# Kernel tuning notes

Hardware: AMD Instinct MI355X
Metric: run time of the kernel (lower is better)

Reference implementation:

```python
import jax, jax.numpy as jnp
import numpy as np

CROP_H = 14
CROP_W = 14
EXTRAPOLATION_VALUE = 0.0


def setup_inputs() -> dict:
    key = jax.random.key(0)
    k1, k2, k3 = jax.random.split(key, 3)
    image = jax.random.normal(k1, (8, 256, 100, 152), dtype=jnp.float32)
    # normalized box coords in [0,1]; (y1,x1,y2,x2), y2<y1 allowed (extrapolation handles it)
    boxes = jax.random.uniform(k2, (1000, 4), dtype=jnp.float32)
    box_ind = jax.random.randint(k3, (1000,), 0, 8, dtype=jnp.int32)
    return {"image": image, "boxes": boxes, "box_ind": box_ind}


def _crop_and_resize(image, boxes, box_ind):
    # image: [B, C, H, W]; boxes: [N, 4] (y1, x1, y2, x2) normalized; box_ind: [N]
    B, C, H, W = image.shape
    dt = image.dtype
    y1, x1, y2, x2 = boxes[:, 0], boxes[:, 1], boxes[:, 2], boxes[:, 3]

    # TF crop_and_resize sampling grid (crop size > 1 path)
    h_scale = (y2 - y1) * (H - 1) / (CROP_H - 1)          # [N]
    w_scale = (x2 - x1) * (W - 1) / (CROP_W - 1)          # [N]
    in_y = y1[:, None] * (H - 1) + jnp.arange(CROP_H, dtype=dt)[None, :] * h_scale[:, None]  # [N, ch]
    in_x = x1[:, None] * (W - 1) + jnp.arange(CROP_W, dtype=dt)[None, :] * w_scale[:, None]  # [N, cw]

    valid_y = (in_y >= 0) & (in_y <= H - 1)               # [N, ch]
    valid_x = (in_x >= 0) & (in_x <= W - 1)               # [N, cw]

    top = jnp.floor(in_y)
    left = jnp.floor(in_x)
    y_lerp = in_y - top                                    # [N, ch]
    x_lerp = in_x - left                                   # [N, cw]

    ti = jnp.clip(top, 0, H - 1).astype(jnp.int32)         # top index    [N, ch]
    bi = jnp.clip(top + 1, 0, H - 1).astype(jnp.int32)     # bottom index [N, ch]
    li = jnp.clip(left, 0, W - 1).astype(jnp.int32)        # left index   [N, cw]
    ri = jnp.clip(left + 1, 0, W - 1).astype(jnp.int32)    # right index  [N, cw]

    b = box_ind[:, None, None]                             # [N, 1, 1]
    yt = ti[:, :, None]
    yb = bi[:, :, None]
    xl = li[:, None, :]
    xr = ri[:, None, :]

    # mixed advanced indexing -> gathered dims first: [N, ch, cw, C]
    tl = image[b, :, yt, xl]
    tr = image[b, :, yt, xr]
    bl = image[b, :, yb, xl]
    br = image[b, :, yb, xr]

    xw = x_lerp[:, None, :, None]                          # [N, 1, cw, 1]
    yw = y_lerp[:, :, None, None]                          # [N, ch, 1, 1]
    top_v = tl + (tr - tl) * xw
    bot_v = bl + (br - bl) * xw
    val = top_v + (bot_v - top_v) * yw                     # [N, ch, cw, C]

    valid = (valid_y[:, :, None] & valid_x[:, None, :])[..., None]
    out = jnp.where(valid, val, jnp.asarray(EXTRAPOLATION_VALUE, dt))
    return jnp.transpose(out, (0, 3, 1, 2))                # [N, C, ch, cw]


def reference(image, boxes, box_ind):
    return _crop_and_resize(image, boxes, box_ind)
```

## Files before the change

### kernel.cpp

```cpp
#include <hip/hip_runtime.h>

#define CROP_H 14
#define CROP_W 14
#define IMG_B 8
#define IMG_C 256
#define IMG_H 100
#define IMG_W 152
#define NBOX 1000
#define PLANE (IMG_H * IMG_W)
#define POS (CROP_H * CROP_W)
#define OUT_PER_BOX (IMG_C * POS)
#define BOXCAP 256
#define CG 32
#define NCG (IMG_C / CG)

typedef float f2u __attribute__((ext_vector_type(2), aligned(4)));

__global__ __launch_bounds__(1024) void sort_boxes_kernel(
    const int* __restrict__ box_ind,
    int* __restrict__ perm,
    int* __restrict__ offsets)
{
    __shared__ unsigned s_mask[IMG_B][32];
    __shared__ int s_tot[IMG_B];
    const int tid = threadIdx.x;

    if (tid < IMG_B * 32) ((unsigned*)s_mask)[tid] = 0u;
    __syncthreads();

    int key = 0;
    if (tid < NBOX) {
        key = box_ind[tid];
        atomicOr(&s_mask[key][tid >> 5], 1u << (tid & 31));
    }
    __syncthreads();

    if (tid < IMG_B) {
        int t = 0;
        #pragma unroll
        for (int w = 0; w < 32; ++w) t += __popc(s_mask[tid][w]);
        s_tot[tid] = t;
    }
    __syncthreads();

    if (tid == 0) {
        int acc = 0;
        #pragma unroll
        for (int k = 0; k < IMG_B; ++k) { offsets[k] = acc; acc += s_tot[k]; }
        offsets[IMG_B] = acc;
    }

    if (tid < NBOX) {
        int base = 0;
        #pragma unroll
        for (int k = 0; k < IMG_B; ++k) base += (k < key) ? s_tot[k] : 0;
        const int w = tid >> 5, b = tid & 31;
        int r = __popc(s_mask[key][w] & ((b == 0) ? 0u : ((1u << b) - 1u)));
        for (int ww = 0; ww < w; ++ww) r += __popc(s_mask[key][ww]);
        perm[base + r] = tid;
    }
}

__global__ __launch_bounds__(512, 4) void CropAndResize_16630113370849_kernel(
    const float* __restrict__ image,
    const float* __restrict__ boxes,
    const int* __restrict__ perm,
    const int* __restrict__ offsets,
    float* __restrict__ out)
{
    __shared__ __align__(16) float s_plane[PLANE];
    __shared__ float s_hs[BOXCAP], s_ws[BOXCAP], s_y1H[BOXCAP], s_x1W[BOXCAP];
    __shared__ int   s_n[BOXCAP];

    const int c   = blockIdx.x;
    const int b   = blockIdx.y;
    const int tid = threadIdx.x;

    {
        const float4* __restrict__ src =
            (const float4*)(image + ((size_t)b * IMG_C + c) * PLANE);
        float4* dst = (float4*)s_plane;
        #pragma unroll
        for (int i = 0; i < 8; ++i) {
            const int e = i * 512 + tid;
            if (e < PLANE / 4) dst[e] = src[e];
        }
    }

    const int s0 = offsets[b], s1 = offsets[b + 1];

    for (int ck = s0; ck < s1; ck += BOXCAP) {
        const int cnt = min(BOXCAP, s1 - ck);

        __syncthreads();
        if (tid < cnt) {
            const int n = perm[ck + tid];
            const float y1 = boxes[n * 4 + 0];
            const float x1 = boxes[n * 4 + 1];
            const float y2 = boxes[n * 4 + 2];
            const float x2 = boxes[n * 4 + 3];
            s_hs[tid]  = __fdiv_rn(__fmul_rn(__fsub_rn(y2, y1), (float)(IMG_H - 1)),
                                   (float)(CROP_H - 1));
            s_ws[tid]  = __fdiv_rn(__fmul_rn(__fsub_rn(x2, x1), (float)(IMG_W - 1)),
                                   (float)(CROP_W - 1));
            s_y1H[tid] = __fmul_rn(y1, (float)(IMG_H - 1));
            s_x1W[tid] = __fmul_rn(x1, (float)(IMG_W - 1));
            s_n[tid]   = n;
        }
        __syncthreads();

        const int total = cnt * POS;
        #pragma unroll 2
        for (int idx = tid; idx < total; idx += 512) {
            const int slot = idx / POS;
            const int p    = idx - slot * POS;
            const int y    = p / CROP_W;
            const int x    = p - y * CROP_W;

            const float in_y = __fadd_rn(s_y1H[slot],
                                         __fmul_rn((float)y, s_hs[slot]));
            const int vy = (in_y >= 0.0f) && (in_y <= (float)(IMG_H - 1));
            const float top = floorf(in_y);
            const float yw  = __fsub_rn(in_y, top);
            const int ti = (int)fminf(fmaxf(top, 0.0f), (float)(IMG_H - 1));

            const float in_x = __fadd_rn(s_x1W[slot],
                                         __fmul_rn((float)x, s_ws[slot]));
            const int vx = (in_x >= 0.0f) && (in_x <= (float)(IMG_W - 1));
            const float left = floorf(in_x);
            const float xw   = __fsub_rn(in_x, left);
            const int li = (int)fminf(fmaxf(left, 0.0f), (float)(IMG_W - 1));

            const int r0 = min(ti, IMG_H - 2);
            const int c0 = min(li, IMG_W - 2);
            const bool sely = (ti == IMG_H - 1);
            const bool selx = (li == IMG_W - 1);
            const bool vald = (vy & vx) != 0;

            const int off = r0 * IMG_W + c0;
            const float a0 = s_plane[off];
            const float a1 = s_plane[off + 1];
            const float b0 = s_plane[off + IMG_W];
            const float b1 = s_plane[off + IMG_W + 1];

            const float tA = sely ? b0 : a0;
            const float tB = sely ? b1 : a1;
            const float tl = selx ? tB : tA;
            const float bl = selx ? b1 : b0;

            const float top_v = __fadd_rn(tl, __fmul_rn(__fsub_rn(tB, tl), xw));
            const float bot_v = __fadd_rn(bl, __fmul_rn(__fsub_rn(b1, bl), xw));
            const float v = __fadd_rn(top_v, __fmul_rn(__fsub_rn(bot_v, top_v), yw));

            out[(size_t)s_n[slot] * OUT_PER_BOX + c * POS + p] = vald ? v : 0.0f;
        }
    }
}

__global__ __launch_bounds__(256) void crop_chw_kernel(
    const float* __restrict__ image,
    const float* __restrict__ boxes,
    const int* __restrict__ box_ind,
    float* __restrict__ out)
{
    const int bid  = blockIdx.x;
    const int cg   = bid & 7;
    const int n    = bid >> 3;
    const int tid  = threadIdx.x;
    if (tid >= POS) return;

    const int b = box_ind[n];
    const int y = tid / CROP_W;
    const int x = tid - y * CROP_W;

    const float y1 = boxes[n * 4 + 0];
    const float x1 = boxes[n * 4 + 1];
    const float y2 = boxes[n * 4 + 2];
    const float x2 = boxes[n * 4 + 3];

    const float hs   = __fdiv_rn(__fmul_rn(__fsub_rn(y2, y1), (float)(IMG_H - 1)),
                                 (float)(CROP_H - 1));
    const float in_y = __fadd_rn(__fmul_rn(y1, (float)(IMG_H - 1)),
                                 __fmul_rn((float)y, hs));
    const int vy = (in_y >= 0.0f) && (in_y <= (float)(IMG_H - 1));
    const float top = floorf(in_y);
    const float yw  = __fsub_rn(in_y, top);
    const int ti = (int)fminf(fmaxf(top, 0.0f), (float)(IMG_H - 1));

    const float ws   = __fdiv_rn(__fmul_rn(__fsub_rn(x2, x1), (float)(IMG_W - 1)),
                                 (float)(CROP_W - 1));
    const float in_x = __fadd_rn(__fmul_rn(x1, (float)(IMG_W - 1)),
                                 __fmul_rn((float)x, ws));
    const int vx = (in_x >= 0.0f) && (in_x <= (float)(IMG_W - 1));
    const float left = floorf(in_x);
    const float xw   = __fsub_rn(in_x, left);
    const int li = (int)fminf(fmaxf(left, 0.0f), (float)(IMG_W - 1));

    const int r0 = min(ti, IMG_H - 2);
    const int c0 = min(li, IMG_W - 2);
    const bool sely = (ti == IMG_H - 1);
    const bool selx = (li == IMG_W - 1);
    const bool vald = (vy & vx) != 0;

    const float* __restrict__ pl =
        image + (size_t)b * (size_t)(IMG_C * PLANE)
              + (size_t)(cg * CG) * PLANE + (r0 * IMG_W + c0);
    float* __restrict__ po =
        out + (size_t)n * (size_t)OUT_PER_BOX + (size_t)(cg * CG) * POS + tid;

    #pragma unroll 8
    for (int cl = 0; cl < CG; ++cl) {
        const f2u ra = *(const f2u*)(pl);
        const f2u rb = *(const f2u*)(pl + IMG_W);
        const float tA = sely ? rb.x : ra.x;
        const float tB = sely ? rb.y : ra.y;
        const float tl = selx ? tB : tA;
        const float bl = selx ? rb.y : rb.x;
        const float top_v = __fadd_rn(tl, __fmul_rn(__fsub_rn(tB, tl), xw));
        const float bot_v = __fadd_rn(bl, __fmul_rn(__fsub_rn(rb.y, bl), xw));
        const float v = __fadd_rn(top_v, __fmul_rn(__fsub_rn(bot_v, top_v), yw));
        *po = vald ? v : 0.0f;
        pl += PLANE;
        po += POS;
    }
}

extern "C" void kernel_launch(void* const* d_in, const int* in_sizes, int n_in,
                              void* d_out, int out_size, void* d_ws, size_t ws_size,
                              hipStream_t stream) {
    const float* image  = (const float*)d_in[0];
    const float* boxes  = (const float*)d_in[1];
    const int*   boxind = (const int*)d_in[2];
    float* out = (float*)d_out;

    const size_t need = (NBOX + IMG_B + 1) * sizeof(int);
    if (ws_size >= need) {
        int* perm    = (int*)d_ws;
        int* offsets = perm + NBOX;

        sort_boxes_kernel<<<1, 1024, 0, stream>>>(boxind, perm, offsets);
        CropAndResize_16630113370849_kernel<<<dim3(IMG_C, IMG_B), 512, 0, stream>>>(
            image, boxes, perm, offsets, out);
    } else {
        crop_chw_kernel<<<dim3(NBOX * NCG), 256, 0, stream>>>(
            image, boxes, boxind, out);
    }
}
```

Baseline: 101.4 us.

## Precompute per-box row/column sampling tables in LDS and widen blocks to 1024 threads

Per chunk of boxes, the kernel now precomputes per-row and per-column sample data (packed index, clamp-select and validity flags plus the lerp weight) into shared tables once per box. The inner loop no longer repeats the coordinate math for each of the 196 output positions. Blocks grow from 512 to 1024 threads and the box chunk shrinks to 64, which adds chunk iterations and barriers. Output offsets use 32-bit unsigned arithmetic, which fits because the whole output is about 50M elements.

```diff
diff --git a/kernel.cpp b/kernel.cpp
--- a/kernel.cpp
+++ b/kernel.cpp
@@ -10,7 +10,7 @@
 #define PLANE (IMG_H * IMG_W)
 #define POS (CROP_H * CROP_W)
 #define OUT_PER_BOX (IMG_C * POS)
-#define BOXCAP 256
+#define BOXCAP 64
 #define CG 32
 #define NCG (IMG_C / CG)
 
@@ -61,7 +61,7 @@
     }
 }
 
-__global__ __launch_bounds__(512, 4) void CropAndResize_16630113370849_kernel(
+__global__ __launch_bounds__(1024, 8) void CropAndResize_16630113370849_kernel(
     const float* __restrict__ image,
     const float* __restrict__ boxes,
     const int* __restrict__ perm,
@@ -69,8 +69,9 @@
     float* __restrict__ out)
 {
     __shared__ __align__(16) float s_plane[PLANE];
-    __shared__ float s_hs[BOXCAP], s_ws[BOXCAP], s_y1H[BOXCAP], s_x1W[BOXCAP];
-    __shared__ int   s_n[BOXCAP];
+    __shared__ f2u s_row[BOXCAP * CROP_H];
+    __shared__ f2u s_col[BOXCAP * CROP_W];
+    __shared__ unsigned s_ob[BOXCAP];
 
     const int c   = blockIdx.x;
     const int b   = blockIdx.y;
@@ -81,78 +82,94 @@
             (const float4*)(image + ((size_t)b * IMG_C + c) * PLANE);
         float4* dst = (float4*)s_plane;
         #pragma unroll
-        for (int i = 0; i < 8; ++i) {
-            const int e = i * 512 + tid;
+        for (int i = 0; i < 4; ++i) {
+            const int e = i * 1024 + tid;
             if (e < PLANE / 4) dst[e] = src[e];
         }
     }
 
     const int s0 = offsets[b], s1 = offsets[b + 1];
+    const unsigned cPOS = (unsigned)(c * POS);
 
     for (int ck = s0; ck < s1; ck += BOXCAP) {
         const int cnt = min(BOXCAP, s1 - ck);
 
         __syncthreads();
-        if (tid < cnt) {
-            const int n = perm[ck + tid];
+
+        for (int j = tid; j < cnt * 28; j += 1024) {
+            const int slot = j / 28;
+            const int t    = j - slot * 28;
+            const int n    = perm[ck + slot];
+            if (t == 0) s_ob[slot] = (unsigned)(n * OUT_PER_BOX);
+
             const float y1 = boxes[n * 4 + 0];
             const float x1 = boxes[n * 4 + 1];
             const float y2 = boxes[n * 4 + 2];
             const float x2 = boxes[n * 4 + 3];
-            s_hs[tid]  = __fdiv_rn(__fmul_rn(__fsub_rn(y2, y1), (float)(IMG_H - 1)),
-                                   (float)(CROP_H - 1));
-            s_ws[tid]  = __fdiv_rn(__fmul_rn(__fsub_rn(x2, x1), (float)(IMG_W - 1)),
-                                   (float)(CROP_W - 1));
-            s_y1H[tid] = __fmul_rn(y1, (float)(IMG_H - 1));
-            s_x1W[tid] = __fmul_rn(x1, (float)(IMG_W - 1));
-            s_n[tid]   = n;
+
+            if (t < CROP_H) {
+                const float hs   = __fdiv_rn(__fmul_rn(__fsub_rn(y2, y1), (float)(IMG_H - 1)),
+                                             (float)(CROP_H - 1));
+                const float in_y = __fadd_rn(__fmul_rn(y1, (float)(IMG_H - 1)),
+                                             __fmul_rn((float)t, hs));
+                const int vy = (in_y >= 0.0f) && (in_y <= (float)(IMG_H - 1));
+                const float top = floorf(in_y);
+                const float yw  = __fsub_rn(in_y, top);
+                const int ti = (int)fminf(fmaxf(top, 0.0f), (float)(IMG_H - 1));
+                const int r0 = min(ti, IMG_H - 2);
+                const int sely = (ti == IMG_H - 1);
+                f2u e; e.x = __int_as_float((r0 * IMG_W) | (sely << 14) | (vy << 15));
+                e.y = yw;
+                s_row[slot * CROP_H + t] = e;
+            } else {
+                const int x = t - CROP_H;
+                const float ws   = __fdiv_rn(__fmul_rn(__fsub_rn(x2, x1), (float)(IMG_W - 1)),
+                                             (float)(CROP_W - 1));
+                const float in_x = __fadd_rn(__fmul_rn(x1, (float)(IMG_W - 1)),
+                                             __fmul_rn((float)x, ws));
+                const int vx = (in_x >= 0.0f) && (in_x <= (float)(IMG_W - 1));
+                const float left = floorf(in_x);
+                const float xw   = __fsub_rn(in_x, left);
+                const int li = (int)fminf(fmaxf(left, 0.0f), (float)(IMG_W - 1));
+                const int c0 = min(li, IMG_W - 2);
+                const int selx = (li == IMG_W - 1);
+                f2u e; e.x = __int_as_float(c0 | (selx << 8) | (vx << 9));
+                e.y = xw;
+                s_col[slot * CROP_W + x] = e;
+            }
         }
         __syncthreads();
 
         const int total = cnt * POS;
         #pragma unroll 2
-        for (int idx = tid; idx < total; idx += 512) {
+        for (int idx = tid; idx < total; idx += 1024) {
             const int slot = idx / POS;
             const int p    = idx - slot * POS;
             const int y    = p / CROP_W;
             const int x    = p - y * CROP_W;
 
-            const float in_y = __fadd_rn(s_y1H[slot],
-                                         __fmul_rn((float)y, s_hs[slot]));
-            const int vy = (in_y >= 0.0f) && (in_y <= (float)(IMG_H - 1));
-            const float top = floorf(in_y);
-            const float yw  = __fsub_rn(in_y, top);
-            const int ti = (int)fminf(fmaxf(top, 0.0f), (float)(IMG_H - 1));
-
-            const float in_x = __fadd_rn(s_x1W[slot],
-                                         __fmul_rn((float)x, s_ws[slot]));
-            const int vx = (in_x >= 0.0f) && (in_x <= (float)(IMG_W - 1));
-            const float left = floorf(in_x);
-            const float xw   = __fsub_rn(in_x, left);
-            const int li = (int)fminf(fmaxf(left, 0.0f), (float)(IMG_W - 1));
-
-            const int r0 = min(ti, IMG_H - 2);
-            const int c0 = min(li, IMG_W - 2);
-            const bool sely = (ti == IMG_H - 1);
-            const bool selx = (li == IMG_W - 1);
-            const bool vald = (vy & vx) != 0;
-
-            const int off = r0 * IMG_W + c0;
+            const f2u re = s_row[slot * CROP_H + y];
+            const f2u ce = s_col[slot * CROP_W + x];
+            const int ri = __float_as_int(re.x);
+            const int ci = __float_as_int(ce.x);
+
+            const int off = (ri & 0x3FFF) + (ci & 0xFF);
             const float a0 = s_plane[off];
             const float a1 = s_plane[off + 1];
             const float b0 = s_plane[off + IMG_W];
             const float b1 = s_plane[off + IMG_W + 1];
 
-            const float tA = sely ? b0 : a0;
-            const float tB = sely ? b1 : a1;
-            const float tl = selx ? tB : tA;
-            const float bl = selx ? b1 : b0;
-
-            const float top_v = __fadd_rn(tl, __fmul_rn(__fsub_rn(tB, tl), xw));
-            const float bot_v = __fadd_rn(bl, __fmul_rn(__fsub_rn(b1, bl), xw));
-            const float v = __fadd_rn(top_v, __fmul_rn(__fsub_rn(bot_v, top_v), yw));
-
-            out[(size_t)s_n[slot] * OUT_PER_BOX + c * POS + p] = vald ? v : 0.0f;
+            const float tA = (ri & 0x4000) ? b0 : a0;
+            const float tB = (ri & 0x4000) ? b1 : a1;
+            const float tl = (ci & 0x100)  ? tB : tA;
+            const float bl = (ci & 0x100)  ? b1 : b0;
+
+            const float top_v = __fadd_rn(tl, __fmul_rn(__fsub_rn(tB, tl), ce.y));
+            const float bot_v = __fadd_rn(bl, __fmul_rn(__fsub_rn(b1, bl), ce.y));
+            const float v = __fadd_rn(top_v, __fmul_rn(__fsub_rn(bot_v, top_v), re.y));
+
+            const bool vald = (ri & 0x8000) && (ci & 0x200);
+            out[(size_t)(s_ob[slot] + cPOS + (unsigned)p)] = vald ? v : 0.0f;
         }
     }
 }
@@ -239,7 +256,7 @@
         int* offsets = perm + NBOX;
 
         sort_boxes_kernel<<<1, 1024, 0, stream>>>(boxind, perm, offsets);
-        CropAndResize_16630113370849_kernel<<<dim3(IMG_C, IMG_B), 512, 0, stream>>>(
+        CropAndResize_16630113370849_kernel<<<dim3(IMG_C, IMG_B), 1024, 0, stream>>>(
             image, boxes, perm, offsets, out);
     } else {
         crop_chw_kernel<<<dim3(NBOX * NCG), 256, 0, stream>>>(
```

Result: slower. 110.1 us (+8.6%).
